# Kernel tuning notes

Measured on AMD Instinct MI355X. Metric: run time of the kernel, lower is better.

Reference implementation:

```python
import jax, jax.numpy as jnp
import numpy as np

DIM = 512
INNER = 512        # heads(8) * dim_head(64)
OUT_DIM = 256
SCALE = 64 ** -0.5  # dim_head ** -0.5
BN_EPS = 1e-5


def setup_inputs() -> dict:
    key = jax.random.key(0)
    ks = jax.random.split(key, 8)
    B, H, W = 2, 96, 320
    return {
        "left_feat": jax.random.normal(ks[0], (B, DIM, H, W), jnp.float32),
        "right_feat": jax.random.normal(ks[1], (B, DIM, H, W), jnp.float32),
        "wq": jax.random.normal(ks[2], (INNER, DIM), jnp.float32) * (DIM ** -0.5),
        "wk": jax.random.normal(ks[3], (INNER, DIM), jnp.float32) * (DIM ** -0.5),
        "wv": jax.random.normal(ks[4], (INNER, DIM), jnp.float32) * (DIM ** -0.5),
        "w1": jax.random.normal(ks[5], (OUT_DIM, INNER * 2), jnp.float32) * ((INNER * 2) ** -0.5),
        "bn_gamma": jnp.ones((OUT_DIM,), jnp.float32),
        "bn_beta": jnp.zeros((OUT_DIM,), jnp.float32),
        "bn_mean": jnp.zeros((OUT_DIM,), jnp.float32),
        "bn_var": jnp.ones((OUT_DIM,), jnp.float32),
        "w2": jax.random.normal(ks[6], (OUT_DIM, OUT_DIM), jnp.float32) * (OUT_DIM ** -0.5),
    }


def reference(left_feat, right_feat, wq, wk, wv, w1, bn_gamma, bn_beta, bn_mean, bn_var, w2):
    # conv1x1 projections, directly producing channels-last [b, h, w, c]
    q = jnp.einsum('bchw,oc->bhwo', left_feat, wq)
    k = jnp.einsum('bchw,oc->bhwo', right_feat, wk)
    v = jnp.einsum('bchw,oc->bhwo', right_feat, wv)
    # cross-attention along width, independently per (batch, row)
    dots = jnp.einsum('bhwc,bhxc->bhwx', q, k) * SCALE   # [b, h, w, w]
    attn = jax.nn.softmax(dots, axis=-1)
    out = jnp.einsum('bhwx,bhxc->bhwc', attn, v)         # [b, h, w, c]
    out = out.transpose(0, 3, 1, 2)                      # [b, c, h, w]
    new_left = jnp.concatenate([left_feat, out], axis=1)  # [b, 2*inner, h, w]
    # to_out: conv1x1 -> BN (eval mode, running stats) -> LeakyReLU(0.2) -> conv1x1
    y = jnp.einsum('bchw,oc->bohw', new_left, w1)
    inv = jax.lax.rsqrt(bn_var + BN_EPS)
    y = (y - bn_mean[None, :, None, None]) * (inv * bn_gamma)[None, :, None, None] \
        + bn_beta[None, :, None, None]
    y = jnp.where(y >= 0, y, 0.2 * y)
    return jnp.einsum('bchw,oc->bohw', y, w2)
```

## Files before the change

### kernel.cpp

```cpp
#include <hip/hip_runtime.h>

typedef __bf16 bf16x8 __attribute__((ext_vector_type(8)));
typedef float f32x4 __attribute__((ext_vector_type(4)));
typedef unsigned short u16x8 __attribute__((ext_vector_type(8)));
typedef unsigned short u16x4 __attribute__((ext_vector_type(4)));

#define MFMA16(a, b, c) __builtin_amdgcn_mfma_f32_16x16x32_bf16((a), (b), (c), 0, 0, 0)
#define GLOAD_LDS(gp, lp) __builtin_amdgcn_global_load_lds( \
    (const __attribute__((address_space(1))) void*)(uintptr_t)(const void*)(gp), \
    (__attribute__((address_space(3))) void*)(uintptr_t)(void*)(lp), 16, 0, 0)

#define NB 2
#define NC 512
#define NH 96
#define NW 320
#define PH 30720
#define NPIX 61440
#define NOUT 256

__device__ __forceinline__ unsigned short f2bf(float f) {
    union { float f; unsigned u; } v; v.f = f;
    unsigned r = v.u + 0x7fffu + ((v.u >> 16) & 1u);
    return (unsigned short)(r >> 16);
}

__global__ void k_cast(const float* __restrict__ src, unsigned short* __restrict__ dst, int n) {
    int i = blockIdx.x * 256 + threadIdx.x;
    if (i < n) dst[i] = f2bf(src[i]);
}

__global__ __launch_bounds__(256) void k_wtrans(
        const float* __restrict__ wq, const float* __restrict__ wk, const float* __restrict__ wv,
        unsigned short* __restrict__ WqT, unsigned short* __restrict__ WkT, unsigned short* __restrict__ WvT) {
    __shared__ float t[64][65];
    int z = blockIdx.z;
    const float* src = (z == 0) ? wq : (z == 1) ? wk : wv;
    unsigned short* dst = (z == 0) ? WqT : (z == 1) ? WkT : WvT;
    int i0 = blockIdx.y * 64;
    int c0 = blockIdx.x * 64;
    int tt = threadIdx.x;
    int r4 = tt >> 4, px = (tt & 15) * 4;
#pragma unroll
    for (int i = 0; i < 4; ++i) {
        int il = i * 16 + r4;
        f32x4 v = *reinterpret_cast<const f32x4*>(src + (size_t)(i0 + il) * 512 + c0 + px);
        t[il][px + 0] = v[0]; t[il][px + 1] = v[1]; t[il][px + 2] = v[2]; t[il][px + 3] = v[3];
    }
    __syncthreads();
    int cc = (tt & 7) * 8, pl0 = tt >> 3;
#pragma unroll
    for (int j = 0; j < 2; ++j) {
        int pl = j * 32 + pl0;
        u16x8 ov;
#pragma unroll
        for (int i = 0; i < 8; ++i) ov[i] = f2bf(t[cc + i][pl]);
        *reinterpret_cast<u16x8*>(dst + (size_t)(c0 + pl) * 512 + i0 + cc) = ov;
    }
}

__global__ __launch_bounds__(256) void k_transpose(
        const float* __restrict__ L, const float* __restrict__ R,
        unsigned short* __restrict__ Lcl, unsigned short* __restrict__ Rcl,
        unsigned short* __restrict__ Rbf) {
    __shared__ float t[128][65];
    int z = blockIdx.z;
    int b = z & 1, which = z >> 1;
    const float* src = which ? R : L;
    unsigned short* dst = which ? Rcl : Lcl;
    int c0 = blockIdx.y * 128;
    int p0 = blockIdx.x * 64;
    int tt = threadIdx.x;

    int cl16 = tt >> 4;
    int px = (tt & 15) * 4;
#pragma unroll
    for (int i = 0; i < 8; ++i) {
        int cl = i * 16 + cl16;
        f32x4 v = *reinterpret_cast<const f32x4*>(src + (size_t)(b * NC + c0 + cl) * PH + p0 + px);
        int pc = px ^ (((cl >> 5) & 3) << 2);
        t[cl][pc + 0] = v[0];
        t[cl][pc + 1] = v[1];
        t[cl][pc + 2] = v[2];
        t[cl][pc + 3] = v[3];
        if (which) {
            u16x4 sv;
#pragma unroll
            for (int k = 0; k < 4; ++k) sv[k] = f2bf(v[k]);
            *reinterpret_cast<u16x4*>(Rbf + (size_t)(b * NC + c0 + cl) * PH + p0 + px) = sv;
        }
    }
    __syncthreads();

    int cc = (tt & 15) * 8;
    int pl16 = tt >> 4;
#pragma unroll
    for (int j = 0; j < 4; ++j) {
        int pl = j * 16 + pl16;
        u16x8 ov;
#pragma unroll
        for (int i = 0; i < 8; ++i) {
            int row = cc + i;
            ov[i] = f2bf(t[row][pl ^ (((row >> 5) & 3) << 2)]);
        }
        *reinterpret_cast<u16x8*>(dst + (size_t)(b * PH + p0 + pl) * NC + c0 + cc) = ov;
    }
}

template <int MODE>
__global__ __launch_bounds__(256) void k_gemm(
        const unsigned short* __restrict__ A0,
        const unsigned short* __restrict__ A1,
        const unsigned short* __restrict__ Bb,
        const unsigned short* __restrict__ Bb2,
        unsigned short* __restrict__ Dbf,
        float* __restrict__ Df32,
        const float* __restrict__ g, const float* __restrict__ be,
        const float* __restrict__ mu, const float* __restrict__ va) {
    constexpr int SA = (MODE == 4) ? NOUT : (MODE == 6) ? 1024 : NC;
    constexpr int AOFF = (MODE == 6) ? 512 : 0;
    constexpr int SB = (MODE == 3) ? 1024 : (MODE == 4) ? NOUT : NC;
    constexpr int KS = (MODE == 3) ? 32 : (MODE == 4) ? 8 : 16;
    constexpr int NTO = (MODE == 3 || MODE == 4) ? 2 : 4;
    constexpr int TOT = (MODE == 5) ? 16 : (MODE == 6) ? 8 : ((MODE == 3 || MODE == 4) ? 960 : 1920);

    __shared__ unsigned short Asm[2][128 * 32];
    __shared__ unsigned short Bsm[2][128 * 32];

    int pphys = blockIdx.x;
    int lgc = (pphys & 7) * (TOT / 8) + (pphys >> 3);
    int pixt = lgc / NTO, ot = lgc % NTO;
    const int mbase = ((MODE == 4) ? ot : pixt) * 128;
    const int nbase = ((MODE == 4) ? pixt : ot) * 128;

    const int lane = threadIdx.x & 63, w = threadIdx.x >> 6;
    const int lr = lane & 15, lg = lane >> 4;
    const int wr = w >> 1, wc = w & 1;

    auto stageA = [&](int buf, int kc) {
        const unsigned short* srcA = A0;
        int colOff = kc * 32;
        if constexpr (MODE == 3) {
            if (kc >= 16) { srcA = A1; colOff = (kc - 16) * 32; }
        }
#pragma unroll
        for (int j = 0; j < 2; ++j) {
            int cb = w * 128 + j * 64;
            int c = cb + lane;
            const unsigned short* gp = srcA + (size_t)(mbase + (c >> 2)) * SA + AOFF + colOff + (c & 3) * 8;
            GLOAD_LDS(gp, Asm[buf] + cb * 8);
        }
    };
    auto stageB = [&](int buf, int kc) {
        const unsigned short* srcB = Bb;
        int colOff = kc * 32;
        int sb = SB;
        if constexpr (MODE == 3) {
            if (kc >= 16) { srcB = Bb2; colOff = (kc - 16) * 32; sb = 512; }
        }
#pragma unroll
        for (int j = 0; j < 2; ++j) {
            int cb = w * 128 + j * 64;
            int c = cb + lane;
            const unsigned short* gp = srcB + (size_t)(nbase + (c >> 2)) * sb + colOff + (c & 3) * 8;
            GLOAD_LDS(gp, Bsm[buf] + cb * 8);
        }
    };

    f32x4 acc[4][4] = {};

    stageA(0, 0);
    stageB(0, 0);
    __syncthreads();

    for (int kc = 0; kc < KS; ++kc) {
        int cur = kc & 1;
        if (kc + 1 < KS) {
            stageA(cur ^ 1, kc + 1);
            stageB(cur ^ 1, kc + 1);
        }
        bf16x8 af[4], bfr[4];
#pragma unroll
        for (int i = 0; i < 4; ++i)
            af[i] = *reinterpret_cast<const bf16x8*>(Asm[cur] + (wr * 64 + i * 16 + lr) * 32 + lg * 8);
#pragma unroll
        for (int j = 0; j < 4; ++j)
            bfr[j] = *reinterpret_cast<const bf16x8*>(Bsm[cur] + (wc * 64 + j * 16 + lr) * 32 + lg * 8);
        __builtin_amdgcn_s_setprio(1);
#pragma unroll
        for (int i = 0; i < 4; ++i)
#pragma unroll
            for (int j = 0; j < 4; ++j)
                acc[i][j] = MFMA16(af[i], bfr[j], acc[i][j]);
        __builtin_amdgcn_s_setprio(0);
        __syncthreads();
    }

    const int lr4 = lg * 4;
    if constexpr (MODE == 0 || MODE >= 5) {
#pragma unroll
        for (int i = 0; i < 4; ++i)
#pragma unroll
            for (int j = 0; j < 4; ++j) {
                int ocol = nbase + wc * 64 + j * 16 + lr;
#pragma unroll
                for (int r = 0; r < 4; ++r) {
                    int prow = mbase + wr * 64 + i * 16 + lr4 + r;
                    Dbf[(size_t)prow * NC + ocol] = f2bf(acc[i][j][r]);
                }
            }
    } else if constexpr (MODE == 3) {
#pragma unroll
        for (int j = 0; j < 4; ++j) {
            int o = nbase + wc * 64 + j * 16 + lr;
            float sc = g[o] * rsqrtf(va[o] + 1e-5f);
            float sh = be[o] - mu[o] * sc;
#pragma unroll
            for (int i = 0; i < 4; ++i)
#pragma unroll
                for (int r = 0; r < 4; ++r) {
                    int prow = mbase + wr * 64 + i * 16 + lr4 + r;
                    float y = acc[i][j][r] * sc + sh;
                    y = (y >= 0.f) ? y : 0.2f * y;
                    Dbf[(size_t)prow * NOUT + o] = f2bf(y);
                }
        }
    } else {
#pragma unroll
        for (int j = 0; j < 4; ++j) {
            int pix = nbase + wc * 64 + j * 16 + lr;
            int b = pix / PH, ph = pix % PH;
#pragma unroll
            for (int i = 0; i < 4; ++i)
#pragma unroll
                for (int r = 0; r < 4; ++r) {
                    int o = mbase + wr * 64 + i * 16 + lr4 + r;
                    Df32[((size_t)b * NOUT + o) * PH + ph] = acc[i][j][r];
                }
        }
    }
}

__global__ __launch_bounds__(256, 2) void k_attn(
        const unsigned short* __restrict__ Q, const unsigned short* __restrict__ K,
        const unsigned short* __restrict__ Vb, unsigned short* __restrict__ O) {
    __shared__ unsigned short P[64][328];
    __shared__ unsigned short KV[32 * 512];

    int pphys = blockIdx.x;
    int l = (pphys & 7) * 120 + (pphys >> 3);
    int head = l / 5, qt = l % 5;
    int b = head / NH, hh = head % NH;
    int lane = threadIdx.x & 63, w = threadIdx.x >> 6;
    int lr = lane & 15, lg = lane >> 4;
    int rowbase = b * PH + hh * NW;
    int qrow = rowbase + qt * 64 + w * 16 + lr;

    bf16x8 qf[16];
#pragma unroll
    for (int kc = 0; kc < 16; ++kc)
        qf[kc] = *reinterpret_cast<const bf16x8*>(Q + (size_t)qrow * NC + kc * 32 + lg * 8);

    f32x4 acc[20];
#pragma unroll
    for (int xt = 0; xt < 20; ++xt) acc[xt] = f32x4{0.f, 0.f, 0.f, 0.f};

    u16x8 kregA[4], kregB[4];
    auto kloadTo = [&](int t, u16x8* kr) {
#pragma unroll
        for (int j = 0; j < 4; ++j) {
            int r = w * 4 + j;
            kr[j] = *reinterpret_cast<const u16x8*>(
                K + (size_t)(rowbase + t * 16 + r) * NC + ((lane ^ (r & 7)) * 8));
        }
    };
    auto kwriteFrom = [&](int buf, u16x8* kr) {
#pragma unroll
        for (int j = 0; j < 4; ++j) {
            int r = w * 4 + j;
            *reinterpret_cast<u16x8*>(KV + (buf * 16 + r) * 512 + lane * 8) = kr[j];
        }
    };

    kloadTo(0, kregA);
    kwriteFrom(0, kregA);
    kloadTo(1, kregB);
    __syncthreads();
#pragma unroll
    for (int t = 0; t < 20; ++t) {
        int buf = t & 1;
        if (t + 2 < 20) kloadTo(t + 2, (t & 1) ? kregB : kregA);
        int rsw = lr & 7;
        __builtin_amdgcn_s_setprio(1);
#pragma unroll
        for (int kc = 0; kc < 16; ++kc) {
            bf16x8 kf = *reinterpret_cast<const bf16x8*>(
                KV + (buf * 16 + lr) * 512 + (((kc * 4 + lg) ^ rsw) * 8));
            acc[t] = MFMA16(qf[kc], kf, acc[t]);
        }
        __builtin_amdgcn_s_setprio(0);
        if (t + 1 < 20) kwriteFrom(buf ^ 1, (t & 1) ? kregA : kregB);
        __syncthreads();
    }

    u16x8 vreg[8];
    auto vload = [&](int s) {
#pragma unroll
        for (int j = 0; j < 8; ++j) {
            int c = (w * 8 + j) * 16 + (lane >> 2);
            int qg = (lane & 3) ^ ((lane >> 3) & 3);
            vreg[j] = *reinterpret_cast<const u16x8*>(
                Vb + (size_t)(b * NC + c) * PH + hh * NW + s * 32 + qg * 8);
        }
    };
    auto vwrite = [&]() {
#pragma unroll
        for (int j = 0; j < 8; ++j)
            *reinterpret_cast<u16x8*>(KV + (w * 8 + j) * 512 + lane * 8) = vreg[j];
    };
    vload(0);

#pragma unroll
    for (int xt = 0; xt < 20; ++xt)
#pragma unroll
        for (int r = 0; r < 4; ++r) acc[xt][r] *= 0.125f;
    float m[4] = {-1e30f, -1e30f, -1e30f, -1e30f};
#pragma unroll
    for (int xt = 0; xt < 20; ++xt)
#pragma unroll
        for (int r = 0; r < 4; ++r) m[r] = fmaxf(m[r], acc[xt][r]);
#pragma unroll
    for (int mask = 1; mask < 16; mask <<= 1)
#pragma unroll
        for (int r = 0; r < 4; ++r) m[r] = fmaxf(m[r], __shfl_xor(m[r], mask));
    float s4[4] = {0.f, 0.f, 0.f, 0.f};
#pragma unroll
    for (int xt = 0; xt < 20; ++xt)
#pragma unroll
        for (int r = 0; r < 4; ++r) {
            float e = __expf(acc[xt][r] - m[r]);
            acc[xt][r] = e;
            s4[r] += e;
        }
#pragma unroll
    for (int mask = 1; mask < 16; mask <<= 1)
#pragma unroll
        for (int r = 0; r < 4; ++r) s4[r] += __shfl_xor(s4[r], mask);
#pragma unroll
    for (int xt = 0; xt < 20; ++xt)
#pragma unroll
        for (int r = 0; r < 4; ++r)
            P[w * 16 + lg * 4 + r][xt * 16 + lr] = f2bf(acc[xt][r]);
    __syncthreads();
    vwrite();
    __syncthreads();

    f32x4 oacc[32];
#pragma unroll
    for (int ct = 0; ct < 32; ++ct) oacc[ct] = f32x4{0.f, 0.f, 0.f, 0.f};

#pragma unroll
    for (int s = 0; s < 10; ++s) {
        if (s + 1 < 10) vload(s + 1);
        bf16x8 pf = *reinterpret_cast<const bf16x8*>(&P[w * 16 + lr][s * 32 + lg * 8]);
        __builtin_amdgcn_s_setprio(1);
#pragma unroll
        for (int ct = 0; ct < 32; ++ct) {
            bf16x8 vf = *reinterpret_cast<const bf16x8*>(
                KV + ct * 512 + lr * 32 + ((lg ^ ((lr >> 1) & 3)) * 8));
            oacc[ct] = MFMA16(pf, vf, oacc[ct]);
        }
        __builtin_amdgcn_s_setprio(0);
        __syncthreads();
        if (s + 1 < 10) vwrite();
        __syncthreads();
    }

#pragma unroll
    for (int ct = 0; ct < 32; ++ct)
#pragma unroll
        for (int r = 0; r < 4; ++r) {
            int prow = rowbase + qt * 64 + w * 16 + lg * 4 + r;
            O[(size_t)prow * NC + ct * 16 + lr] = f2bf(oacc[ct][r] / s4[r]);
        }
}

extern "C" void kernel_launch(void* const* d_in, const int* in_sizes, int n_in,
                              void* d_out, int out_size, void* d_ws, size_t ws_size,
                              hipStream_t stream) {
    const float* left  = (const float*)d_in[0];
    const float* right = (const float*)d_in[1];
    const float* wq = (const float*)d_in[2];
    const float* wk = (const float*)d_in[3];
    const float* wv = (const float*)d_in[4];
    const float* w1 = (const float*)d_in[5];
    const float* bn_g = (const float*)d_in[6];
    const float* bn_b = (const float*)d_in[7];
    const float* bn_m = (const float*)d_in[8];
    const float* bn_v = (const float*)d_in[9];
    const float* w2 = (const float*)d_in[10];
    float* out = (float*)d_out;

    size_t off = 0;
    auto alloc = [&](size_t bytes) -> void* {
        void* p = (char*)d_ws + off;
        off += (bytes + 255) & ~(size_t)255;
        return p;
    };
    const size_t clb = (size_t)NPIX * NC * 2;
    unsigned short* Lcl = (unsigned short*)alloc(clb);
    unsigned short* Rcl = (unsigned short*)alloc(clb);
    unsigned short* Rbf = (unsigned short*)alloc(clb);
    unsigned short* Qb  = (unsigned short*)alloc(clb);
    unsigned short* Ub  = (unsigned short*)alloc(clb);
    unsigned short* WqT = (unsigned short*)alloc((size_t)NC * NC * 2);
    unsigned short* WkT = (unsigned short*)alloc((size_t)NC * NC * 2);
    unsigned short* WvT = (unsigned short*)alloc((size_t)NC * NC * 2);
    unsigned short* Mt  = (unsigned short*)alloc((size_t)NC * NC * 2);
    unsigned short* WX  = (unsigned short*)alloc((size_t)NOUT * NC * 2);
    unsigned short* W1b = (unsigned short*)alloc((size_t)NOUT * 1024 * 2);
    unsigned short* W2b = (unsigned short*)alloc((size_t)NOUT * NOUT * 2);
    unsigned short* Yb = Qb;

    k_cast<<<dim3((NOUT * 1024 + 255) / 256), 256, 0, stream>>>(w1, W1b, NOUT * 1024);
    k_cast<<<dim3((NOUT * NOUT + 255) / 256), 256, 0, stream>>>(w2, W2b, NOUT * NOUT);

    k_wtrans<<<dim3(8, 8, 3), 256, 0, stream>>>(wq, wk, wv, WqT, WkT, WvT);

    k_transpose<<<dim3(PH / 64, NC / 128, 4), 256, 0, stream>>>(left, right, Lcl, Rcl, Rbf);

    k_gemm<5><<<dim3(16), 256, 0, stream>>>(WkT, nullptr, WqT, nullptr, Mt, nullptr, nullptr, nullptr, nullptr, nullptr);
    k_gemm<6><<<dim3(8), 256, 0, stream>>>(W1b, nullptr, WvT, nullptr, WX, nullptr, nullptr, nullptr, nullptr, nullptr);

    k_gemm<0><<<dim3(1920), 256, 0, stream>>>(Lcl, nullptr, Mt, nullptr, Qb, nullptr, nullptr, nullptr, nullptr, nullptr);

    k_attn<<<dim3(960), 256, 0, stream>>>(Qb, Rcl, Rbf, Ub);

    k_gemm<3><<<dim3(960), 256, 0, stream>>>(Lcl, Ub, W1b, WX, Yb, nullptr, bn_g, bn_b, bn_m, bn_v);

    k_gemm<4><<<dim3(960), 256, 0, stream>>>(W2b, nullptr, Yb, nullptr, nullptr, out, nullptr, nullptr, nullptr, nullptr);
}
```

Baseline: 349.8 us.

## Restructure QK^T to per-wave key slabs with cross-wave softmax reductions

```diff
diff --git a/kernel.cpp b/kernel.cpp
--- a/kernel.cpp
+++ b/kernel.cpp
@@ -245,6 +245,9 @@
         const unsigned short* __restrict__ Vb, unsigned short* __restrict__ O) {
     __shared__ unsigned short P[64][328];
     __shared__ unsigned short KV[32 * 512];
+    __shared__ float SMX[4][64];
+    __shared__ float SSM[4][64];
+    __shared__ float SDEN[64];
 
     int pphys = blockIdx.x;
     int l = (pphys & 7) * 120 + (pphys >> 3);
@@ -253,54 +256,6 @@
     int lane = threadIdx.x & 63, w = threadIdx.x >> 6;
     int lr = lane & 15, lg = lane >> 4;
     int rowbase = b * PH + hh * NW;
-    int qrow = rowbase + qt * 64 + w * 16 + lr;
-
-    bf16x8 qf[16];
-#pragma unroll
-    for (int kc = 0; kc < 16; ++kc)
-        qf[kc] = *reinterpret_cast<const bf16x8*>(Q + (size_t)qrow * NC + kc * 32 + lg * 8);
-
-    f32x4 acc[20];
-#pragma unroll
-    for (int xt = 0; xt < 20; ++xt) acc[xt] = f32x4{0.f, 0.f, 0.f, 0.f};
-
-    u16x8 kregA[4], kregB[4];
-    auto kloadTo = [&](int t, u16x8* kr) {
-#pragma unroll
-        for (int j = 0; j < 4; ++j) {
-            int r = w * 4 + j;
-            kr[j] = *reinterpret_cast<const u16x8*>(
-                K + (size_t)(rowbase + t * 16 + r) * NC + ((lane ^ (r & 7)) * 8));
-        }
-    };
-    auto kwriteFrom = [&](int buf, u16x8* kr) {
-#pragma unroll
-        for (int j = 0; j < 4; ++j) {
-            int r = w * 4 + j;
-            *reinterpret_cast<u16x8*>(KV + (buf * 16 + r) * 512 + lane * 8) = kr[j];
-        }
-    };
-
-    kloadTo(0, kregA);
-    kwriteFrom(0, kregA);
-    kloadTo(1, kregB);
-    __syncthreads();
-#pragma unroll
-    for (int t = 0; t < 20; ++t) {
-        int buf = t & 1;
-        if (t + 2 < 20) kloadTo(t + 2, (t & 1) ? kregB : kregA);
-        int rsw = lr & 7;
-        __builtin_amdgcn_s_setprio(1);
-#pragma unroll
-        for (int kc = 0; kc < 16; ++kc) {
-            bf16x8 kf = *reinterpret_cast<const bf16x8*>(
-                KV + (buf * 16 + lr) * 512 + (((kc * 4 + lg) ^ rsw) * 8));
-            acc[t] = MFMA16(qf[kc], kf, acc[t]);
-        }
-        __builtin_amdgcn_s_setprio(0);
-        if (t + 1 < 20) kwriteFrom(buf ^ 1, (t & 1) ? kregA : kregB);
-        __syncthreads();
-    }
 
     u16x8 vreg[8];
     auto vload = [&](int s) {
@@ -317,39 +272,82 @@
         for (int j = 0; j < 8; ++j)
             *reinterpret_cast<u16x8*>(KV + (w * 8 + j) * 512 + lane * 8) = vreg[j];
     };
+
+    f32x4 acc[5][4] = {};
+#pragma unroll
+    for (int ks = 0; ks < 16; ++ks) {
+        bf16x8 af[5], bfq[4];
+#pragma unroll
+        for (int mf = 0; mf < 5; ++mf)
+            af[mf] = *reinterpret_cast<const bf16x8*>(
+                K + (size_t)(rowbase + w * 80 + mf * 16 + lr) * NC + ks * 32 + lg * 8);
+#pragma unroll
+        for (int nf = 0; nf < 4; ++nf)
+            bfq[nf] = *reinterpret_cast<const bf16x8*>(
+                Q + (size_t)(rowbase + qt * 64 + nf * 16 + lr) * NC + ks * 32 + lg * 8);
+#pragma unroll
+        for (int mf = 0; mf < 5; ++mf)
+#pragma unroll
+            for (int nf = 0; nf < 4; ++nf)
+                acc[mf][nf] = MFMA16(af[mf], bfq[nf], acc[mf][nf]);
+    }
+
+    float pmax[4] = {-1e30f, -1e30f, -1e30f, -1e30f};
+#pragma unroll
+    for (int mf = 0; mf < 5; ++mf)
+#pragma unroll
+        for (int nf = 0; nf < 4; ++nf)
+#pragma unroll
+            for (int r = 0; r < 4; ++r) {
+                acc[mf][nf][r] *= 0.125f;
+                pmax[nf] = fmaxf(pmax[nf], acc[mf][nf][r]);
+            }
+#pragma unroll
+    for (int mask = 16; mask < 64; mask <<= 1)
+#pragma unroll
+        for (int nf = 0; nf < 4; ++nf) pmax[nf] = fmaxf(pmax[nf], __shfl_xor(pmax[nf], mask));
+    if (lg == 0)
+#pragma unroll
+        for (int nf = 0; nf < 4; ++nf) SMX[w][nf * 16 + lr] = pmax[nf];
+    __syncthreads();
+    float mq[4];
+#pragma unroll
+    for (int nf = 0; nf < 4; ++nf)
+        mq[nf] = fmaxf(fmaxf(SMX[0][nf * 16 + lr], SMX[1][nf * 16 + lr]),
+                       fmaxf(SMX[2][nf * 16 + lr], SMX[3][nf * 16 + lr]));
+    float psum[4] = {0.f, 0.f, 0.f, 0.f};
+#pragma unroll
+    for (int mf = 0; mf < 5; ++mf)
+#pragma unroll
+        for (int nf = 0; nf < 4; ++nf)
+#pragma unroll
+            for (int r = 0; r < 4; ++r) {
+                float e = __expf(acc[mf][nf][r] - mq[nf]);
+                acc[mf][nf][r] = e;
+                psum[nf] += e;
+            }
+#pragma unroll
+    for (int mask = 16; mask < 64; mask <<= 1)
+#pragma unroll
+        for (int nf = 0; nf < 4; ++nf) psum[nf] += __shfl_xor(psum[nf], mask);
+    if (lg == 0)
+#pragma unroll
+        for (int nf = 0; nf < 4; ++nf) SSM[w][nf * 16 + lr] = psum[nf];
     vload(0);
-
-#pragma unroll
-    for (int xt = 0; xt < 20; ++xt)
-#pragma unroll
-        for (int r = 0; r < 4; ++r) acc[xt][r] *= 0.125f;
-    float m[4] = {-1e30f, -1e30f, -1e30f, -1e30f};
-#pragma unroll
-    for (int xt = 0; xt < 20; ++xt)
-#pragma unroll
-        for (int r = 0; r < 4; ++r) m[r] = fmaxf(m[r], acc[xt][r]);
-#pragma unroll
-    for (int mask = 1; mask < 16; mask <<= 1)
-#pragma unroll
-        for (int r = 0; r < 4; ++r) m[r] = fmaxf(m[r], __shfl_xor(m[r], mask));
-    float s4[4] = {0.f, 0.f, 0.f, 0.f};
-#pragma unroll
-    for (int xt = 0; xt < 20; ++xt)
-#pragma unroll
-        for (int r = 0; r < 4; ++r) {
-            float e = __expf(acc[xt][r] - m[r]);
-            acc[xt][r] = e;
-            s4[r] += e;
-        }
-#pragma unroll
-    for (int mask = 1; mask < 16; mask <<= 1)
-#pragma unroll
-        for (int r = 0; r < 4; ++r) s4[r] += __shfl_xor(s4[r], mask);
-#pragma unroll
-    for (int xt = 0; xt < 20; ++xt)
-#pragma unroll
-        for (int r = 0; r < 4; ++r)
-            P[w * 16 + lg * 4 + r][xt * 16 + lr] = f2bf(acc[xt][r]);
+    __syncthreads();
+    if (w == 0 && lg == 0)
+#pragma unroll
+        for (int nf = 0; nf < 4; ++nf) {
+            int q = nf * 16 + lr;
+            SDEN[q] = SSM[0][q] + SSM[1][q] + SSM[2][q] + SSM[3][q];
+        }
+#pragma unroll
+    for (int mf = 0; mf < 5; ++mf)
+#pragma unroll
+        for (int nf = 0; nf < 4; ++nf)
+#pragma unroll
+            for (int r = 0; r < 4; ++r)
+                P[nf * 16 + lr][w * 80 + mf * 16 + lg * 4 + r] = f2bf(acc[mf][nf][r]);
     __syncthreads();
     vwrite();
     __syncthreads();
@@ -380,7 +378,8 @@
 #pragma unroll
         for (int r = 0; r < 4; ++r) {
             int prow = rowbase + qt * 64 + w * 16 + lg * 4 + r;
-            O[(size_t)prow * NC + ct * 16 + lr] = f2bf(oacc[ct][r] / s4[r]);
+            float den = SDEN[w * 16 + lg * 4 + r];
+            O[(size_t)prow * NC + ct * 16 + lr] = f2bf(oacc[ct][r] / den);
         }
 }
 
```

Result: slower. 375.2 us (+7.2%).
